# Optimization experiments

Measured on AMD Instinct MI355X. Metric: run time of the kernel, lower is better.

## Reference

```python
import jax, jax.numpy as jnp
import numpy as np

THRESH = 0.5
DECAY = 0.2
N_NODES = 39
T = 2000
K_HOPS = 3


def setup_inputs() -> dict:
    key = jax.random.key(0)
    ks = jax.random.split(key, 10)
    x = jax.random.normal(ks[0], (N_NODES, 2, T), dtype=jnp.float32)
    edge_index = jax.random.randint(ks[1], (2, 156), 0, N_NODES)
    # TAGConv(2, 64, K=3): (K+1) bias-free hop weights + single bias
    W_conv = jax.random.normal(ks[2], (K_HOPS + 1, 2, 64), dtype=jnp.float32) * 0.3
    b_conv = jax.random.normal(ks[3], (64,), dtype=jnp.float32) * 0.05
    W1 = jax.random.normal(ks[4], (N_NODES * 64, 128), dtype=jnp.float32) * 0.02
    b1 = jax.random.normal(ks[5], (128,), dtype=jnp.float32) * 0.02
    W2 = jax.random.normal(ks[6], (128, 256), dtype=jnp.float32) * 0.08
    b2 = jax.random.normal(ks[7], (256,), dtype=jnp.float32) * 0.02
    W3 = jax.random.normal(ks[8], (256, 36), dtype=jnp.float32) * 0.06
    b3 = jax.random.normal(ks[9], (36,), dtype=jnp.float32) * 0.02
    return {"x": x, "edge_index": edge_index, "W_conv": W_conv, "b_conv": b_conv,
            "W1": W1, "b1": b1, "W2": W2, "b2": b2, "W3": W3, "b3": b3}


def _norm_adj(edge_index, dtype):
    # PyG gcn_norm without self loops: A_hat = D^-1/2 A D^-1/2, message flows row->col
    row, col = edge_index[0], edge_index[1]
    A = jnp.zeros((N_NODES, N_NODES), dtype).at[col, row].add(1.0)
    deg = A.sum(axis=1)
    dinv = jnp.where(deg > 0, deg ** -0.5, 0.0).astype(dtype)
    return dinv[:, None] * A * dinv[None, :]


def reference(x, edge_index, W_conv, b_conv, W1, b1, W2, b2, W3, b3):
    A_hat = _norm_adj(edge_index, x.dtype)

    def spike(m):
        return (m > THRESH).astype(m.dtype)

    def step(carry, xt):
        c1m, c1s, h1m, h1s, h2m, h2s, h3m, h3s, acc = carry
        # TAGConv: sum_k (A_hat^k xt) @ W_k + bias   [39,64]
        h = xt
        conv = h @ W_conv[0]
        for k in range(1, K_HOPS + 1):
            h = A_hat @ h
            conv = conv + h @ W_conv[k]
        conv = conv + b_conv
        c1m = c1m * DECAY * (1.0 - c1s) + conv
        c1s = spike(c1m)
        f = c1s.reshape(-1)  # [2496]
        h1m = h1m * DECAY * (1.0 - h1s) + f @ W1 + b1
        h1s = spike(h1m)
        h2m = h2m * DECAY * (1.0 - h2s) + h1s @ W2 + b2
        h2s = spike(h2m)
        h3m = h3m * DECAY * (1.0 - h3s) + h2s @ W3 + b3
        h3s = spike(h3m)
        return (c1m, c1s, h1m, h1s, h2m, h2s, h3m, h3s, acc + h3s), None

    z = lambda s: jnp.zeros(s, x.dtype)
    init = (z((N_NODES, 64)), z((N_NODES, 64)), z((128,)), z((128,)),
            z((256,)), z((256,)), z((36,)), z((36,)), z((36,)))
    xs = jnp.moveaxis(x, -1, 0)  # [T, 39, 2]
    carry, _ = jax.lax.scan(step, init, xs)
    return carry[-1] / x.shape[-1]
```

## Files before the change

### kernel.cpp

```cpp
#include <hip/hip_runtime.h>

#define T 2000
#define K1N 2496
#define K2 4992
#define TLA 8
#define MAXNZ 24
#define NBLK 250
#define S2P 420

using short8 = __attribute__((ext_vector_type(8))) short;
using floatx4 = __attribute__((ext_vector_type(4))) float;

__device__ __forceinline__ unsigned bf16_rne(float v) {
    unsigned u = __float_as_uint(v);
    return (u + 0x7FFFu + ((u >> 16) & 1u)) >> 16;
}
__device__ __forceinline__ unsigned packhl(float w) {
    unsigned hi = bf16_rne(w);
    float r = w - __uint_as_float(hi << 16);
    unsigned lo = bf16_rne(r);
    return (hi & 0xFFFFu) | (lo << 16);
}
__device__ __forceinline__ short8 spike8(unsigned u) {
    union { uint4 d; short8 s; } r;
    r.d.x = (u & 0x000000FFu) ? 0x3F803F80u : 0u;
    r.d.y = (u & 0x0000FF00u) ? 0x3F803F80u : 0u;
    r.d.z = (u & 0x00FF0000u) ? 0x3F803F80u : 0u;
    r.d.w = (u & 0xFF000000u) ? 0x3F803F80u : 0u;
    return r.s;
}

__global__ __launch_bounds__(256) void hops(const float* __restrict__ x,
        const int* __restrict__ ei, float* __restrict__ Fg,
        const float* __restrict__ W1, unsigned* __restrict__ W1t,
        float* __restrict__ out) {
    __shared__ float ah[1560];
    __shared__ float2 alist[39 * MAXNZ];
    __shared__ int nnzr[40];
    __shared__ float bufA[78 * TLA];
    __shared__ float bufB[78 * TLA];
    __shared__ float feat[39 * TLA * 8];
    int tid = threadIdx.x;
    int bl = blockIdx.x;
    int ts = bl * TLA;

    if (bl == 0 && tid < 36) out[tid] = 0.f;

    for (int u = tid; u < 1521; u += 256) ah[u] = 0.f;
    __syncthreads();
    if (tid < 156) atomicAdd(&ah[ei[156 + tid] * 39 + ei[tid]], 1.f);
    __syncthreads();
    if (tid < 39) {
        float d = 0.f;
        for (int u = 0; u < 39; ++u) d += ah[tid * 39 + u];
        ah[1521 + tid] = (d > 0.f) ? (1.f / sqrtf(d)) : 0.f;
    }
    __syncthreads();
    for (int u = tid; u < 1521; u += 256) {
        int i = u / 39, j = u - i * 39;
        ah[u] = (ah[1521 + i] * ah[u]) * ah[1521 + j];
    }
    __syncthreads();
    if (tid < 39) {
        int cnt = 0;
        for (int m = 0; m < 39; ++m) {
            float v = ah[tid * 39 + m];
            if (v != 0.f && cnt < MAXNZ) {
                alist[tid * MAXNZ + cnt] = make_float2(v, __int_as_float((2 * m) * TLA * 4));
                ++cnt;
            }
        }
        nnzr[tid] = cnt;
    }
    __syncthreads();

    for (int e = tid; e < 78 * TLA; e += 256) {
        int r = e / TLA, tt = e - r * TLA;
        bufA[r * TLA + tt] = x[r * T + ts + tt];
    }
    __syncthreads();

    for (int e = tid; e < 78 * TLA; e += 256) {
        int r = e / TLA, tt = e - r * TLA;
        feat[((r >> 1) * TLA + tt) * 8 + (r & 1)] = bufA[r * TLA + tt];
    }
    for (int e = tid; e < 78; e += 256) {
        int r = e, ii = r >> 1, c = r & 1;
        float acc[8];
        #pragma unroll
        for (int u = 0; u < 8; ++u) acc[u] = 0.f;
        int nz = nnzr[ii];
        const float2* lp = &alist[ii * MAXNZ];
        int cg = c * (TLA * 4);
        for (int q = 0; q < nz; ++q) {
            float2 av = lp[q];
            const float* xp = (const float*)((const char*)bufA + (__float_as_int(av.y) + cg));
            float a = av.x;
            float4 x0 = *(const float4*)xp;
            float4 x1 = *(const float4*)(xp + 4);
            acc[0] += a * x0.x; acc[1] += a * x0.y; acc[2] += a * x0.z; acc[3] += a * x0.w;
            acc[4] += a * x1.x; acc[5] += a * x1.y; acc[6] += a * x1.z; acc[7] += a * x1.w;
        }
        float* dp = &bufB[r * TLA];
        *(float4*)dp = *(float4*)&acc[0];
        *(float4*)(dp + 4) = *(float4*)&acc[4];
    }
    __syncthreads();

    for (int e = tid; e < 78 * TLA; e += 256) {
        int r = e / TLA, tt = e - r * TLA;
        feat[((r >> 1) * TLA + tt) * 8 + 2 + (r & 1)] = bufB[r * TLA + tt];
    }
    for (int e = tid; e < 78; e += 256) {
        int r = e, ii = r >> 1, c = r & 1;
        float acc[8];
        #pragma unroll
        for (int u = 0; u < 8; ++u) acc[u] = 0.f;
        int nz = nnzr[ii];
        const float2* lp = &alist[ii * MAXNZ];
        int cg = c * (TLA * 4);
        for (int q = 0; q < nz; ++q) {
            float2 av = lp[q];
            const float* xp = (const float*)((const char*)bufB + (__float_as_int(av.y) + cg));
            float a = av.x;
            float4 x0 = *(const float4*)xp;
            float4 x1 = *(const float4*)(xp + 4);
            acc[0] += a * x0.x; acc[1] += a * x0.y; acc[2] += a * x0.z; acc[3] += a * x0.w;
            acc[4] += a * x1.x; acc[5] += a * x1.y; acc[6] += a * x1.z; acc[7] += a * x1.w;
        }
        float* dp = &bufA[r * TLA];
        *(float4*)dp = *(float4*)&acc[0];
        *(float4*)(dp + 4) = *(float4*)&acc[4];
    }
    __syncthreads();

    for (int e = tid; e < 78 * TLA; e += 256) {
        int r = e / TLA, tt = e - r * TLA;
        feat[((r >> 1) * TLA + tt) * 8 + 4 + (r & 1)] = bufA[r * TLA + tt];
    }
    for (int e = tid; e < 78; e += 256) {
        int r = e, ii = r >> 1, c = r & 1;
        float acc[8];
        #pragma unroll
        for (int u = 0; u < 8; ++u) acc[u] = 0.f;
        int nz = nnzr[ii];
        const float2* lp = &alist[ii * MAXNZ];
        int cg = c * (TLA * 4);
        for (int q = 0; q < nz; ++q) {
            float2 av = lp[q];
            const float* xp = (const float*)((const char*)bufA + (__float_as_int(av.y) + cg));
            float a = av.x;
            float4 x0 = *(const float4*)xp;
            float4 x1 = *(const float4*)(xp + 4);
            acc[0] += a * x0.x; acc[1] += a * x0.y; acc[2] += a * x0.z; acc[3] += a * x0.w;
            acc[4] += a * x1.x; acc[5] += a * x1.y; acc[6] += a * x1.z; acc[7] += a * x1.w;
        }
        #pragma unroll
        for (int u = 0; u < 8; ++u)
            feat[(ii * TLA + u) * 8 + 6 + c] = acc[u];
    }
    __syncthreads();

    for (int e = tid; e < 39 * TLA * 2; e += 256) {
        int idx = e >> 1, half = e & 1;
        int n = idx / TLA, tt = idx - n * TLA;
        *(float4*)&Fg[((size_t)n * T + ts + tt) * 8 + half * 4] =
            *(const float4*)&feat[idx * 8 + half * 4];
    }

    const int total = 128 * K1N;
    for (int f = bl * 256 + tid; f < total; f += NBLK * 256) {
        int k = f >> 7, jj = f & 127;
        W1t[jj * K1N + k] = packhl(W1[f]);
    }
}

__global__ __launch_bounds__(512) void scan_gemm1(
        const float* __restrict__ Fg, const float* __restrict__ Wc,
        const float* __restrict__ bc, const short* __restrict__ W1t,
        float* __restrict__ F1p) {
    __shared__ __align__(16) char smem[32 * S2P + 10752];
    unsigned char* S2 = (unsigned char*)smem;
    float* FgL = (float*)(smem + 32 * S2P);

    int tid = threadIdx.x;
    int bx = blockIdx.x, ks = blockIdx.y;
    int t0 = bx * 32;
    int hs = t0 - 16; if (hs < 0) hs = 0;
    int ncol = t0 + 32 - hs;
    int k0g = ks * 416;
    int nd0 = k0g >> 6;
    int kb2 = ks * 832;

    for (int e = tid; e < 7 * ncol * 2; e += 512) {
        int idx = e >> 1, half = e & 1;
        int nl = idx / ncol, cc = idx - nl * ncol;
        int t = hs + cc;
        int gn = nd0 + nl;
        float4 v = make_float4(0.f, 0.f, 0.f, 0.f);
        if (gn < 39 && t < T)
            v = *(const float4*)&Fg[((size_t)gn * T + t) * 8 + half * 4];
        *(float4*)&FgL[(nl * ncol + cc) * 8 + half * 4] = v;
    }
    __syncthreads();

    {
        int cn = tid;
        if (cn < 416) {
            int gk = k0g + cn;
            int nl = (gk >> 6) - nd0;
            int j = gk & 63;
            float wv[8];
            #pragma unroll
            for (int q = 0; q < 8; ++q) wv[q] = Wc[q * 64 + j];
            float bias = bc[j];
            float m = 0.f, s = 0.f;
            const float* fb = &FgL[nl * ncol * 8];
            for (int cc = 0; cc < ncol; ++cc) {
                float4 a0 = *(const float4*)&fb[cc * 8];
                float4 a1 = *(const float4*)&fb[cc * 8 + 4];
                float acc = 0.f;
                acc += wv[0] * a0.x; acc += wv[1] * a0.y;
                acc += wv[2] * a0.z; acc += wv[3] * a0.w;
                acc += wv[4] * a1.x; acc += wv[5] * a1.y;
                acc += wv[6] * a1.z; acc += wv[7] * a1.w;
                float v = acc + bias;
                m = m * 0.2f * (1.f - s) + v;
                s = (m > 0.5f) ? 1.f : 0.f;
                int t = hs + cc;
                if (t >= t0) S2[(t - t0) * S2P + cn] = (unsigned char)(s != 0.f);
            }
        }
    }
    __syncthreads();

    int lane = tid & 63, wvi = tid >> 6;
    int j0 = wvi * 16;
    int row = lane & 15, quad = lane >> 4;
    floatx4 a00 = {0.f, 0.f, 0.f, 0.f};
    floatx4 a10 = a00;
    const short* wrow = &W1t[(j0 + row) * K2 + kb2];
    const unsigned char* s2a = &S2[row * S2P];
    const unsigned char* s2b = &S2[(row + 16) * S2P];
    for (int c = 0; c < 13; ++c) {
        #pragma unroll
        for (int sh = 0; sh < 2; ++sh) {
            int kbyte = c * 32 + sh * 16 + quad * 4;
            unsigned ua0 = *(const unsigned*)&s2a[kbyte];
            unsigned ua1 = *(const unsigned*)&s2b[kbyte];
            short8 fa0 = spike8(ua0);
            short8 fa1 = spike8(ua1);
            short8 fb0 = *(const short8*)&wrow[c * 64 + sh * 32 + quad * 8];
            a00 = __builtin_amdgcn_mfma_f32_16x16x32_bf16(fa0, fb0, a00, 0, 0, 0);
            a10 = __builtin_amdgcn_mfma_f32_16x16x32_bf16(fa1, fb0, a10, 0, 0, 0);
        }
    }
    #pragma unroll
    for (int r = 0; r < 4; ++r) {
        int m0 = quad * 4 + r;
        int t = t0 + m0;
        if (t < T)
            F1p[t * 768 + ks * 128 + j0 + row] = a00[r];
        int t2 = t0 + 16 + m0;
        if (t2 < T)
            F1p[t2 * 768 + ks * 128 + j0 + row] = a10[r];
    }
}

__global__ __launch_bounds__(256) void h1_gemm2(const float* __restrict__ F1p,
        const float* __restrict__ b1, const float* __restrict__ W2,
        float* __restrict__ G2) {
    __shared__ float AT[128 * 8];
    int tid = threadIdx.x;
    int t0 = blockIdx.x * 8;
    if (tid < 128) {
        int n = tid;
        int hs = t0 - 16; if (hs < 0) hs = 0;
        float b = b1[n];
        float m = 0.f, s = 0.f;
        for (int tg = hs; tg < t0 + 8; tg += 4) {
            float vb[4][6];
            #pragma unroll
            for (int u = 0; u < 4; ++u)
                #pragma unroll
                for (int q = 0; q < 6; ++q)
                    vb[u][q] = F1p[(tg + u) * 768 + q * 128 + n];
            #pragma unroll
            for (int u = 0; u < 4; ++u) {
                float v = 0.f;
                #pragma unroll
                for (int q = 0; q < 6; ++q) v += vb[u][q];
                v += b;
                m = m * 0.2f * (1.f - s) + v;
                s = (m > 0.5f) ? 1.f : 0.f;
                int t = tg + u;
                if (t >= t0) AT[n * 8 + (t - t0)] = s;
            }
        }
    }
    __syncthreads();
    int j = tid;
    float acc[8] = {0.f};
    #pragma unroll 4
    for (int k = 0; k < 128; ++k) {
        float w = W2[k * 256 + j];
        float4 q0 = *(const float4*)&AT[k * 8 + 0];
        float4 q1 = *(const float4*)&AT[k * 8 + 4];
        acc[0] += q0.x * w; acc[1] += q0.y * w; acc[2] += q0.z * w; acc[3] += q0.w * w;
        acc[4] += q1.x * w; acc[5] += q1.y * w; acc[6] += q1.z * w; acc[7] += q1.w * w;
    }
    #pragma unroll
    for (int tt = 0; tt < 8; ++tt) G2[(t0 + tt) * 256 + j] = acc[tt];
}

__global__ __launch_bounds__(256) void tail(const float* __restrict__ G2,
        const float* __restrict__ b2, const float* __restrict__ W3,
        const float* __restrict__ b3, float* __restrict__ out) {
    __shared__ float w3t[36 * 260];
    __shared__ unsigned char S2[52 * 260];
    __shared__ float G3[52 * 36];
    int tid = threadIdx.x;
    int t0 = blockIdx.x * 25;
    int gs = t0 - 25; if (gs < 0) gs = 0;
    int hs = gs - 25; if (hs < 0) hs = 0;
    int L3 = t0 + 25 - gs;
    #pragma unroll
    for (int u = 0; u < 9; ++u) {
        int f = u * 1024 + tid * 4;
        float4 wq = *(const float4*)&W3[f];
        int k0 = f / 36, j0 = f - k0 * 36;
        float wv[4] = {wq.x, wq.y, wq.z, wq.w};
        #pragma unroll
        for (int q = 0; q < 4; ++q) {
            int k = (j0 + q >= 36) ? k0 + 1 : k0;
            int jj = (j0 + q >= 36) ? (j0 + q - 36) : (j0 + q);
            w3t[jj * 260 + k] = wv[q];
        }
    }
    {
        int n = tid;
        float b = b2[n];
        float m = 0.f, s = 0.f;
        for (int base = hs; base < t0 + 25; base += 25) {
            float vb[25];
            #pragma unroll
            for (int u = 0; u < 25; ++u) vb[u] = G2[(base + u) * 256 + n];
            #pragma unroll
            for (int u = 0; u < 25; ++u) {
                float v = vb[u] + b;
                m = m * 0.2f * (1.f - s) + v;
                s = (m > 0.5f) ? 1.f : 0.f;
                int t = base + u;
                if (t >= gs) S2[(t - gs) * 260 + n] = (unsigned char)(s != 0.f);
            }
        }
    }
    __syncthreads();
    for (int e = tid; e < 36 * 13; e += 256) {
        int jj = e / 13, g = e - (e / 13) * 13;
        int tb = g * 4;
        if (tb >= L3) continue;
        float ac0 = 0.f, ac1 = 0.f, ac2 = 0.f, ac3 = 0.f;
        const unsigned char* r0 = &S2[tb * 260];
        for (int k = 0; k < 256; k += 4) {
            float4 w = *(const float4*)&w3t[jj * 260 + k];
            uchar4 q0 = *(const uchar4*)&r0[k];
            uchar4 q1 = *(const uchar4*)&r0[260 + k];
            uchar4 q2 = *(const uchar4*)&r0[520 + k];
            uchar4 q3 = *(const uchar4*)&r0[780 + k];
            ac0 += (float)q0.x * w.x + (float)q0.y * w.y + (float)q0.z * w.z + (float)q0.w * w.w;
            ac1 += (float)q1.x * w.x + (float)q1.y * w.y + (float)q1.z * w.z + (float)q1.w * w.w;
            ac2 += (float)q2.x * w.x + (float)q2.y * w.y + (float)q2.z * w.z + (float)q2.w * w.w;
            ac3 += (float)q3.x * w.x + (float)q3.y * w.y + (float)q3.z * w.z + (float)q3.w * w.w;
        }
        G3[tb * 36 + jj] = ac0;
        if (tb + 1 < L3) G3[(tb + 1) * 36 + jj] = ac1;
        if (tb + 2 < L3) G3[(tb + 2) * 36 + jj] = ac2;
        if (tb + 3 < L3) G3[(tb + 3) * 36 + jj] = ac3;
    }
    __syncthreads();
    if (tid < 36) {
        int n = tid;
        float b = b3[n];
        float m = 0.f, s = 0.f;
        int cnt = 0;
        for (int t = gs; t < t0 + 25; ++t) {
            float v = G3[(t - gs) * 36 + n] + b;
            m = m * 0.2f * (1.f - s) + v;
            s = (m > 0.5f) ? 1.f : 0.f;
            if (t >= t0) cnt += (s != 0.f) ? 1 : 0;
        }
        atomicAdd(&out[n], (float)cnt * 0.0005f);
    }
}

extern "C" void kernel_launch(void* const* d_in, const int* in_sizes, int n_in,
                              void* d_out, int out_size, void* d_ws, size_t ws_size,
                              hipStream_t stream) {
    const float* x  = (const float*)d_in[0];
    const int*   ei = (const int*)d_in[1];
    const float* Wc = (const float*)d_in[2];
    const float* bc = (const float*)d_in[3];
    const float* W1 = (const float*)d_in[4];
    const float* b1 = (const float*)d_in[5];
    const float* W2 = (const float*)d_in[6];
    const float* b2 = (const float*)d_in[7];
    const float* W3 = (const float*)d_in[8];
    const float* b3 = (const float*)d_in[9];
    float* out = (float*)d_out;

    float* w = (float*)d_ws;
    float* F1p = w;                       w += (size_t)T * 768;
    float* G2  = w;                       w += (size_t)T * 256;
    float* Fg  = w;                       w += (size_t)39 * T * 8;
    unsigned* W1t = (unsigned*)w;         w += 128 * K1N;

    hops<<<NBLK, 256, 0, stream>>>(x, ei, Fg, W1, W1t, out);
    scan_gemm1<<<dim3(63, 6), 512, 0, stream>>>(Fg, Wc, bc, (const short*)W1t, F1p);
    h1_gemm2<<<250, 256, 0, stream>>>(F1p, b1, W2, G2);
    tail<<<80, 256, 0, stream>>>(G2, b2, W3, b3, out);
}
```

Before: 137.8 us.

## Fuse graph-hop kernel into scan/GEMM1 kernel and pack W1 inline

Merges the hops kernel into scan_gemm1. Each (time-tile, k-slice) block now rebuilds the normalized adjacency and computes the three graph hops for its 48-column window in shared memory, instead of reading a precomputed Fg buffer from global memory. The separate W1 transpose/bf16 hi-lo packing pass is removed, and W1 is loaded and packed directly inside the MFMA loop using strided global loads. This drops one kernel launch and the Fg and W1t round trips through memory. In exchange, every block recomputes the adjacency and all hops redundantly, and the MFMA loop does uncoalesced W1 loads plus packing work.

```diff
diff --git a/kernel.cpp b/kernel.cpp
--- a/kernel.cpp
+++ b/kernel.cpp
@@ -2,10 +2,7 @@
 
 #define T 2000
 #define K1N 2496
-#define K2 4992
-#define TLA 8
 #define MAXNZ 24
-#define NBLK 250
 #define S2P 420
 
 using short8 = __attribute__((ext_vector_type(8))) short;
@@ -30,23 +27,32 @@
     return r.s;
 }
 
-__global__ __launch_bounds__(256) void hops(const float* __restrict__ x,
-        const int* __restrict__ ei, float* __restrict__ Fg,
-        const float* __restrict__ W1, unsigned* __restrict__ W1t,
+__global__ __launch_bounds__(512) void conv_gemm1(
+        const float* __restrict__ x, const int* __restrict__ ei,
+        const float* __restrict__ Wc, const float* __restrict__ bc,
+        const float* __restrict__ W1, float* __restrict__ F1p,
         float* __restrict__ out) {
-    __shared__ float ah[1560];
-    __shared__ float2 alist[39 * MAXNZ];
-    __shared__ int nnzr[40];
-    __shared__ float bufA[78 * TLA];
-    __shared__ float bufB[78 * TLA];
-    __shared__ float feat[39 * TLA * 8];
+    __shared__ __align__(16) char smem[48352];
+    float2* alist = (float2*)smem;
+    int*    nnzr  = (int*)(smem + 7488);
+    float*  bufA  = (float*)(smem + 7648);
+    unsigned char* S2 = (unsigned char*)(smem + 7648);
+    float*  bufB  = (float*)(smem + 22624);
+    float*  ah    = (float*)(smem + 22624);
+    float*  FgL   = (float*)(smem + 37600);
+
     int tid = threadIdx.x;
-    int bl = blockIdx.x;
-    int ts = bl * TLA;
-
-    if (bl == 0 && tid < 36) out[tid] = 0.f;
-
-    for (int u = tid; u < 1521; u += 256) ah[u] = 0.f;
+    int bx = blockIdx.x, ks = blockIdx.y;
+    int t0 = bx * 32;
+    int hs = t0 - 16; if (hs < 0) hs = 0;
+    int ncol = t0 + 32 - hs;
+    int GC = ncol >> 3;
+    int k0g = ks * 416;
+    int nd0 = k0g >> 6;
+
+    if (bx == 0 && ks == 0 && tid < 36) out[tid] = 0.f;
+
+    for (int u = tid; u < 1521; u += 512) ah[u] = 0.f;
     __syncthreads();
     if (tid < 156) atomicAdd(&ah[ei[156 + tid] * 39 + ei[tid]], 1.f);
     __syncthreads();
@@ -56,7 +62,7 @@
         ah[1521 + tid] = (d > 0.f) ? (1.f / sqrtf(d)) : 0.f;
     }
     __syncthreads();
-    for (int u = tid; u < 1521; u += 256) {
+    for (int u = tid; u < 1521; u += 512) {
         int i = u / 39, j = u - i * 39;
         ah[u] = (ah[1521 + i] * ah[u]) * ah[1521 + j];
     }
@@ -66,7 +72,7 @@
         for (int m = 0; m < 39; ++m) {
             float v = ah[tid * 39 + m];
             if (v != 0.f && cnt < MAXNZ) {
-                alist[tid * MAXNZ + cnt] = make_float2(v, __int_as_float((2 * m) * TLA * 4));
+                alist[tid * MAXNZ + cnt] = make_float2(v, __int_as_float((2 * m) * 192));
                 ++cnt;
             }
         }
@@ -74,24 +80,27 @@
     }
     __syncthreads();
 
-    for (int e = tid; e < 78 * TLA; e += 256) {
-        int r = e / TLA, tt = e - r * TLA;
-        bufA[r * TLA + tt] = x[r * T + ts + tt];
-    }
-    __syncthreads();
-
-    for (int e = tid; e < 78 * TLA; e += 256) {
-        int r = e / TLA, tt = e - r * TLA;
-        feat[((r >> 1) * TLA + tt) * 8 + (r & 1)] = bufA[r * TLA + tt];
-    }
-    for (int e = tid; e < 78; e += 256) {
-        int r = e, ii = r >> 1, c = r & 1;
+    for (int e = tid; e < 78 * ncol; e += 512) {
+        int r = e / ncol, cc = e - r * ncol;
+        int t = hs + cc;
+        bufA[r * 48 + cc] = (t < T) ? x[r * T + t] : 0.f;
+    }
+    __syncthreads();
+
+    for (int e = tid; e < 7 * ncol * 2; e += 512) {
+        int c = e & 1, idx = e >> 1;
+        int nl = idx / ncol, cc = idx - nl * ncol;
+        FgL[(nl * ncol + cc) * 8 + c] = bufA[((nd0 + nl) * 2 + c) * 48 + cc];
+    }
+    for (int e = tid; e < 78 * GC; e += 512) {
+        int r = e / GC, g = e - r * GC;
+        int ii = r >> 1, c = r & 1;
         float acc[8];
         #pragma unroll
         for (int u = 0; u < 8; ++u) acc[u] = 0.f;
         int nz = nnzr[ii];
         const float2* lp = &alist[ii * MAXNZ];
-        int cg = c * (TLA * 4);
+        int cg = c * 192 + g * 32;
         for (int q = 0; q < nz; ++q) {
             float2 av = lp[q];
             const float* xp = (const float*)((const char*)bufA + (__float_as_int(av.y) + cg));
@@ -101,24 +110,26 @@
             acc[0] += a * x0.x; acc[1] += a * x0.y; acc[2] += a * x0.z; acc[3] += a * x0.w;
             acc[4] += a * x1.x; acc[5] += a * x1.y; acc[6] += a * x1.z; acc[7] += a * x1.w;
         }
-        float* dp = &bufB[r * TLA];
+        float* dp = &bufB[r * 48 + g * 8];
         *(float4*)dp = *(float4*)&acc[0];
         *(float4*)(dp + 4) = *(float4*)&acc[4];
     }
     __syncthreads();
 
-    for (int e = tid; e < 78 * TLA; e += 256) {
-        int r = e / TLA, tt = e - r * TLA;
-        feat[((r >> 1) * TLA + tt) * 8 + 2 + (r & 1)] = bufB[r * TLA + tt];
-    }
-    for (int e = tid; e < 78; e += 256) {
-        int r = e, ii = r >> 1, c = r & 1;
+    for (int e = tid; e < 7 * ncol * 2; e += 512) {
+        int c = e & 1, idx = e >> 1;
+        int nl = idx / ncol, cc = idx - nl * ncol;
+        FgL[(nl * ncol + cc) * 8 + 2 + c] = bufB[((nd0 + nl) * 2 + c) * 48 + cc];
+    }
+    for (int e = tid; e < 78 * GC; e += 512) {
+        int r = e / GC, g = e - r * GC;
+        int ii = r >> 1, c = r & 1;
         float acc[8];
         #pragma unroll
         for (int u = 0; u < 8; ++u) acc[u] = 0.f;
         int nz = nnzr[ii];
         const float2* lp = &alist[ii * MAXNZ];
-        int cg = c * (TLA * 4);
+        int cg = c * 192 + g * 32;
         for (int q = 0; q < nz; ++q) {
             float2 av = lp[q];
             const float* xp = (const float*)((const char*)bufB + (__float_as_int(av.y) + cg));
@@ -128,24 +139,27 @@
             acc[0] += a * x0.x; acc[1] += a * x0.y; acc[2] += a * x0.z; acc[3] += a * x0.w;
             acc[4] += a * x1.x; acc[5] += a * x1.y; acc[6] += a * x1.z; acc[7] += a * x1.w;
         }
-        float* dp = &bufA[r * TLA];
+        float* dp = &bufA[r * 48 + g * 8];
         *(float4*)dp = *(float4*)&acc[0];
         *(float4*)(dp + 4) = *(float4*)&acc[4];
     }
     __syncthreads();
 
-    for (int e = tid; e < 78 * TLA; e += 256) {
-        int r = e / TLA, tt = e - r * TLA;
-        feat[((r >> 1) * TLA + tt) * 8 + 4 + (r & 1)] = bufA[r * TLA + tt];
-    }
-    for (int e = tid; e < 78; e += 256) {
-        int r = e, ii = r >> 1, c = r & 1;
+    for (int e = tid; e < 7 * ncol * 2; e += 512) {
+        int c = e & 1, idx = e >> 1;
+        int nl = idx / ncol, cc = idx - nl * ncol;
+        FgL[(nl * ncol + cc) * 8 + 4 + c] = bufA[((nd0 + nl) * 2 + c) * 48 + cc];
+    }
+    for (int e = tid; e < 14 * GC; e += 512) {
+        int lr = e / GC, g = e - lr * GC;
+        int il = lr >> 1, c = lr & 1;
+        int gi = nd0 + il;
         float acc[8];
         #pragma unroll
         for (int u = 0; u < 8; ++u) acc[u] = 0.f;
-        int nz = nnzr[ii];
-        const float2* lp = &alist[ii * MAXNZ];
-        int cg = c * (TLA * 4);
+        int nz = nnzr[gi];
+        const float2* lp = &alist[gi * MAXNZ];
+        int cg = c * 192 + g * 32;
         for (int q = 0; q < nz; ++q) {
             float2 av = lp[q];
             const float* xp = (const float*)((const char*)bufA + (__float_as_int(av.y) + cg));
@@ -157,50 +171,7 @@
         }
         #pragma unroll
         for (int u = 0; u < 8; ++u)
-            feat[(ii * TLA + u) * 8 + 6 + c] = acc[u];
-    }
-    __syncthreads();
-
-    for (int e = tid; e < 39 * TLA * 2; e += 256) {
-        int idx = e >> 1, half = e & 1;
-        int n = idx / TLA, tt = idx - n * TLA;
-        *(float4*)&Fg[((size_t)n * T + ts + tt) * 8 + half * 4] =
-            *(const float4*)&feat[idx * 8 + half * 4];
-    }
-
-    const int total = 128 * K1N;
-    for (int f = bl * 256 + tid; f < total; f += NBLK * 256) {
-        int k = f >> 7, jj = f & 127;
-        W1t[jj * K1N + k] = packhl(W1[f]);
-    }
-}
-
-__global__ __launch_bounds__(512) void scan_gemm1(
-        const float* __restrict__ Fg, const float* __restrict__ Wc,
-        const float* __restrict__ bc, const short* __restrict__ W1t,
-        float* __restrict__ F1p) {
-    __shared__ __align__(16) char smem[32 * S2P + 10752];
-    unsigned char* S2 = (unsigned char*)smem;
-    float* FgL = (float*)(smem + 32 * S2P);
-
-    int tid = threadIdx.x;
-    int bx = blockIdx.x, ks = blockIdx.y;
-    int t0 = bx * 32;
-    int hs = t0 - 16; if (hs < 0) hs = 0;
-    int ncol = t0 + 32 - hs;
-    int k0g = ks * 416;
-    int nd0 = k0g >> 6;
-    int kb2 = ks * 832;
-
-    for (int e = tid; e < 7 * ncol * 2; e += 512) {
-        int idx = e >> 1, half = e & 1;
-        int nl = idx / ncol, cc = idx - nl * ncol;
-        int t = hs + cc;
-        int gn = nd0 + nl;
-        float4 v = make_float4(0.f, 0.f, 0.f, 0.f);
-        if (gn < 39 && t < T)
-            v = *(const float4*)&Fg[((size_t)gn * T + t) * 8 + half * 4];
-        *(float4*)&FgL[(nl * ncol + cc) * 8 + half * 4] = v;
+            FgL[(il * ncol + g * 8 + u) * 8 + 6 + c] = acc[u];
     }
     __syncthreads();
 
@@ -239,20 +210,26 @@
     int row = lane & 15, quad = lane >> 4;
     floatx4 a00 = {0.f, 0.f, 0.f, 0.f};
     floatx4 a10 = a00;
-    const short* wrow = &W1t[(j0 + row) * K2 + kb2];
+    int j = j0 + row;
     const unsigned char* s2a = &S2[row * S2P];
     const unsigned char* s2b = &S2[(row + 16) * S2P];
+    const float* w1c = &W1[j];
     for (int c = 0; c < 13; ++c) {
         #pragma unroll
         for (int sh = 0; sh < 2; ++sh) {
             int kbyte = c * 32 + sh * 16 + quad * 4;
             unsigned ua0 = *(const unsigned*)&s2a[kbyte];
             unsigned ua1 = *(const unsigned*)&s2b[kbyte];
+            int k4 = k0g + kbyte;
+            union { uint4 d; short8 s; } fb;
+            fb.d.x = packhl(w1c[(size_t)(k4 + 0) * 128]);
+            fb.d.y = packhl(w1c[(size_t)(k4 + 1) * 128]);
+            fb.d.z = packhl(w1c[(size_t)(k4 + 2) * 128]);
+            fb.d.w = packhl(w1c[(size_t)(k4 + 3) * 128]);
             short8 fa0 = spike8(ua0);
             short8 fa1 = spike8(ua1);
-            short8 fb0 = *(const short8*)&wrow[c * 64 + sh * 32 + quad * 8];
-            a00 = __builtin_amdgcn_mfma_f32_16x16x32_bf16(fa0, fb0, a00, 0, 0, 0);
-            a10 = __builtin_amdgcn_mfma_f32_16x16x32_bf16(fa1, fb0, a10, 0, 0, 0);
+            a00 = __builtin_amdgcn_mfma_f32_16x16x32_bf16(fa0, fb.s, a00, 0, 0, 0);
+            a10 = __builtin_amdgcn_mfma_f32_16x16x32_bf16(fa1, fb.s, a10, 0, 0, 0);
         }
     }
     #pragma unroll
@@ -411,12 +388,9 @@
 
     float* w = (float*)d_ws;
     float* F1p = w;                       w += (size_t)T * 768;
-    float* G2  = w;                       w += (size_t)T * 256;
-    float* Fg  = w;                       w += (size_t)39 * T * 8;
-    unsigned* W1t = (unsigned*)w;         w += 128 * K1N;
-
-    hops<<<NBLK, 256, 0, stream>>>(x, ei, Fg, W1, W1t, out);
-    scan_gemm1<<<dim3(63, 6), 512, 0, stream>>>(Fg, Wc, bc, (const short*)W1t, F1p);
+    float* G2  = w;
+
+    conv_gemm1<<<dim3(63, 6), 512, 0, stream>>>(x, ei, Wc, bc, W1, F1p, out);
     h1_gemm2<<<250, 256, 0, stream>>>(F1p, b1, W2, G2);
     tail<<<80, 256, 0, stream>>>(G2, b2, W3, b3, out);
 }
```

Measured after the change: 138.9 us. Within noise of the previous version (+0.8%).
